# Performance work log

Measured on AMD Instinct MI355X. Metric: run time of the kernel, lower is better.

Reference implementation:

```python
import jax, jax.numpy as jnp
import numpy as np

B, T, C, H = 4, 2048, 768, 12
D = C // H  # head_dim = 64
ROPE_BASE = 10000.0


def _make_rope_cache(seq_len, n_elem, base=ROPE_BASE):
    theta = 1.0 / base ** (jnp.arange(0, n_elem, 2, dtype=jnp.float32) / n_elem)  # [D/2]
    idx_theta = jnp.arange(seq_len, dtype=jnp.float32)[:, None] * theta[None, :]  # [T, D/2]
    return jnp.stack([jnp.cos(idx_theta), jnp.sin(idx_theta)], axis=-1)  # [T, D/2, 2]


def setup_inputs() -> dict:
    key = jax.random.key(0)
    k1, k2, k3 = jax.random.split(key, 3)
    x = jax.random.normal(k1, (B, T, C), dtype=jnp.float32)
    rope_cache = _make_rope_cache(T, D)
    w_qkv = jax.random.normal(k2, (3 * C, C), dtype=jnp.float32) * (1.0 / np.sqrt(C))
    w_o = jax.random.normal(k3, (C, C), dtype=jnp.float32) * (1.0 / np.sqrt(C))
    return {"x": x, "rope_cache": rope_cache, "w_qkv": w_qkv, "w_o": w_o}


def _apply_rope(t, cos, sin):
    # t: [B,T,H,D]; cos/sin: [T,D/2] broadcast to [1,T,1,D/2]
    tp = t.reshape(t.shape[:-1] + (D // 2, 2))
    t0, t1 = tp[..., 0], tp[..., 1]
    c = cos[None, :, None, :]
    s = sin[None, :, None, :]
    rot = jnp.stack([t0 * c - t1 * s, t0 * s + t1 * c], axis=-1)
    return rot.reshape(t.shape)


def reference(x, rope_cache, w_qkv, w_o):
    b, t, c = x.shape
    qkv = (x @ w_qkv.T).reshape(b, t, 3, H, D)
    q, k, v = qkv[:, :, 0], qkv[:, :, 1], qkv[:, :, 2]  # [B,T,H,D]
    cos = rope_cache[:t, :, 0]
    sin = rope_cache[:t, :, 1]
    q = _apply_rope(q, cos, sin)
    k = _apply_rope(k, cos, sin)
    scale = 1.0 / np.sqrt(D)
    att = jnp.einsum('bqhd,bkhd->bhqk', q, k) * scale  # [B,H,T,T]
    causal = jnp.tril(jnp.ones((t, t), dtype=bool))
    att = jnp.where(causal[None, None], att, jnp.finfo(att.dtype).min)
    att = jax.nn.softmax(att, axis=-1)
    y = jnp.einsum('bhqk,bkhd->bqhd', att, v).reshape(b, t, c)
    return y @ w_o.T
```

## Files before the change

kernel.cpp:

```cpp
#include <hip/hip_runtime.h>

#define B_  4
#define T_  2048
#define C_  768
#define H_  12
#define D_  64

typedef unsigned short u16;
typedef unsigned int   u32;
typedef __bf16 bf16;
typedef __bf16 bf16x4 __attribute__((ext_vector_type(4)));
typedef __bf16 bf16x8 __attribute__((ext_vector_type(8)));
typedef float  f32x4  __attribute__((ext_vector_type(4)));
typedef float  f32x16 __attribute__((ext_vector_type(16)));
typedef u32    u32x4  __attribute__((ext_vector_type(4)));
typedef __attribute__((address_space(1))) void* gas_t;
typedef __attribute__((address_space(3))) void* las_t;

static __device__ __forceinline__ u16 f2bf(float f) {
  u32 u = __builtin_bit_cast(u32, f);
  u += 0x7FFFu + ((u >> 16) & 1u);
  return (u16)(u >> 16);
}

static __device__ __forceinline__ u32 cvtpk(float a, float b) {
  u32 r;
  asm("v_cvt_pk_bf16_f32 %0, %1, %2" : "=v"(r) : "v"(a), "v"(b));
  return r;
}
static __device__ __forceinline__ void plswap(u32& a, u32& b) {
  asm volatile("v_permlane32_swap_b32 %0, %1" : "+v"(a), "+v"(b));
}

__global__ __launch_bounds__(256) void k_cvt3(const float* __restrict__ a0,
                                              const float* __restrict__ a1,
                                              const float* __restrict__ a2,
                                              u16* __restrict__ o0,
                                              u16* __restrict__ o1,
                                              u16* __restrict__ o2) {
  const int bid = blockIdx.x;
  const int tid = threadIdx.x;
  if (bid < 6144) {
    const int i = bid * 256 + tid;
    const float4 v = ((const float4*)a0)[i];
    ushort4 o;
    o.x = f2bf(v.x); o.y = f2bf(v.y); o.z = f2bf(v.z); o.w = f2bf(v.w);
    ((ushort4*)o0)[i] = o;
  } else if (bid < 7872) {
    const int i = (bid - 6144) * 256 + tid;
    const int n = i / 192;
    const int c4 = i - n * 192;
    int n2 = n;
    if (n < 1536) {
      const int d = n & 63;
      const int c = (((d & 1) | ((d >> 5) << 1)) << 4) | ((d >> 1) & 15);
      n2 = (n & ~63) | c;
    }
    const float4 v = ((const float4*)a1)[i];
    ushort4 o;
    o.x = f2bf(v.x); o.y = f2bf(v.y); o.z = f2bf(v.z); o.w = f2bf(v.w);
    ((ushort4*)o1)[n2 * 192 + c4] = o;
  } else {
    const int i = (bid - 7872) * 256 + tid;
    const float4 v = ((const float4*)a2)[i];
    ushort4 o;
    o.x = f2bf(v.x); o.y = f2bf(v.y); o.z = f2bf(v.z); o.w = f2bf(v.w);
    ((ushort4*)o2)[i] = o;
  }
}

template<int MODE>
__global__ __launch_bounds__(256) void k_gemm_bt(const u16* __restrict__ A,
                                                 const u16* __restrict__ Bt,
                                                 float* __restrict__ Cout,
                                                 u16* __restrict__ qout,
                                                 u16* __restrict__ kout,
                                                 u16* __restrict__ vout,
                                                 const float* __restrict__ rope,
                                                 int M, int N, int K) {
  __shared__ u16 lA[128 * 32];
  __shared__ u16 lB[128 * 32];
  const int tid = threadIdx.x;
  const int l = tid & 63, w = tid >> 6;
  const int lo = l & 15, hi = l >> 4;
  const int wr = w >> 1, wc = w & 1;
  const int pid = blockIdx.x + gridDim.x * blockIdx.y;
  const int total = gridDim.x * gridDim.y;
  const int lid = (pid & 7) * (total >> 3) + (pid >> 3);
  const int bx = lid % gridDim.x, by = lid / gridDim.x;
  const int m0 = by * 128, n0 = bx * 128;

  f32x4 acc[4][4] = {};
  for (int k0 = 0; k0 < K; k0 += 32) {
#pragma unroll
    for (int r = 0; r < 2; ++r) {
      const int c = tid + 256 * r;
      const int row = c >> 2, cb = (c & 3) * 8;
      __builtin_amdgcn_global_load_lds((gas_t)(u16*)(A + (size_t)(m0 + row) * K + k0 + cb),
                                       (las_t)(lA + c * 8), 16, 0, 0);
      __builtin_amdgcn_global_load_lds((gas_t)(u16*)(Bt + (size_t)(n0 + row) * K + k0 + cb),
                                       (las_t)(lB + c * 8), 16, 0, 0);
    }
    __syncthreads();
    bf16x8 af[4], bfr[4];
#pragma unroll
    for (int i = 0; i < 4; ++i)
      af[i] = *(const bf16x8*)(lA + (wr * 64 + i * 16 + lo) * 32 + hi * 8);
#pragma unroll
    for (int j = 0; j < 4; ++j)
      bfr[j] = *(const bf16x8*)(lB + (wc * 64 + j * 16 + lo) * 32 + hi * 8);
#pragma unroll
    for (int i = 0; i < 4; ++i)
#pragma unroll
      for (int j = 0; j < 4; ++j)
        acc[i][j] = __builtin_amdgcn_mfma_f32_16x16x32_bf16(af[i], bfr[j], acc[i][j], 0, 0, 0);
    __syncthreads();
  }
  const int crow = m0 + wr * 64;
  if (MODE == 1) {
    const int ccol = n0 + wc * 64;
#pragma unroll
    for (int i = 0; i < 4; ++i)
#pragma unroll
      for (int j = 0; j < 4; ++j)
#pragma unroll
        for (int r = 0; r < 4; ++r)
          Cout[(size_t)(crow + i * 16 + hi * 4 + r) * N + ccol + j * 16 + lo] = acc[i][j][r];
  } else {
    const int sect = bx / 6;
    const int h2 = (bx % 6) * 2 + wc;
    if (sect < 2) {
      const float qsc = (sect == 0) ? 0.18033688011f : 1.0f;
      u16* dst = (sect == 0) ? qout : kout;
#pragma unroll
      for (int i = 0; i < 4; ++i)
#pragma unroll
        for (int r = 0; r < 4; ++r) {
          const int trow = crow + i * 16 + hi * 4 + r;
          const int t = trow & (T_ - 1), bb = trow >> 11;
          const float2 cs0 = *(const float2*)(rope + ((size_t)t * 32 + lo) * 2);
          const float2 cs1 = *(const float2*)(rope + ((size_t)t * 32 + 16 + lo) * 2);
          const float a0 = acc[i][0][r], a1 = acc[i][1][r];
          const float a2 = acc[i][2][r], a3 = acc[i][3][r];
          const float e0 = (a0 * cs0.x - a1 * cs0.y) * qsc;
          const float e1 = (a0 * cs0.y + a1 * cs0.x) * qsc;
          const float e2 = (a2 * cs1.x - a3 * cs1.y) * qsc;
          const float e3 = (a2 * cs1.y + a3 * cs1.x) * qsc;
          u16* row = dst + ((size_t)(bb * H_ + h2) * T_ + t) * D_;
          *(ushort2*)(row + 2 * lo)      = make_ushort2(f2bf(e0), f2bf(e1));
          *(ushort2*)(row + 32 + 2 * lo) = make_ushort2(f2bf(e2), f2bf(e3));
        }
    } else {
#pragma unroll
      for (int i = 0; i < 4; ++i)
#pragma unroll
        for (int j = 0; j < 4; ++j)
#pragma unroll
          for (int r = 0; r < 4; ++r) {
            const int trow = crow + i * 16 + hi * 4 + r;
            vout[(size_t)trow * C_ + h2 * D_ + j * 16 + lo] = f2bf(acc[i][j][r]);
          }
    }
  }
}

__global__ __launch_bounds__(256) void k_vtrans(const u16* __restrict__ vtmp,
                                                u16* __restrict__ vt) {
  __shared__ u16 lds[64][68];
  const int bid = blockIdx.x;
  const int ttile = bid & 31, bh = bid >> 5;
  const int b = bh / H_, h = bh % H_;
  const int tid = threadIdx.x;
  const int tl = tid >> 2, doff = (tid & 3) * 16;
  const u16* src = vtmp + (size_t)(b * T_ + ttile * 64 + tl) * C_ + h * D_ + doff;
  const uint4 v0 = *(const uint4*)(src);
  const uint4 v1 = *(const uint4*)(src + 8);
  *(uint2*)&lds[tl][doff + 0]  = make_uint2(v0.x, v0.y);
  *(uint2*)&lds[tl][doff + 4]  = make_uint2(v0.z, v0.w);
  *(uint2*)&lds[tl][doff + 8]  = make_uint2(v1.x, v1.y);
  *(uint2*)&lds[tl][doff + 12] = make_uint2(v1.z, v1.w);
  __syncthreads();
  const int d = tl, toff = doff;
  uint4 o0, o1;
#define PK(j) ((u32)lds[toff + (j)][d] | ((u32)lds[toff + (j) + 1][d] << 16))
  o0.x = PK(0);  o0.y = PK(2);  o0.z = PK(4);  o0.w = PK(6);
  o1.x = PK(8);  o1.y = PK(10); o1.z = PK(12); o1.w = PK(14);
#undef PK
  u16* dst = vt + ((size_t)bh * D_ + d) * T_ + ttile * 64 + toff;
  *(uint4*)(dst) = o0;
  *(uint4*)(dst + 8) = o1;
}

__global__ __launch_bounds__(256) void k_attn(const u16* __restrict__ qb,
                                              const u16* __restrict__ kb,
                                              const u16* __restrict__ vtb,
                                              u16* __restrict__ yb) {
  __shared__ u16 kbuf[2][64 * 64];
  __shared__ u16 vbuf[2][64 * 64];
  const int tid = threadIdx.x;
  const int w = tid >> 6, l = tid & 63;
  const int q5 = l & 31, hf = l >> 5;
  const int pid = blockIdx.x;
  const int xcd = pid & 7;
  const int rank = pid >> 3;
  const int wv = rank >> 5, ps = rank & 31;
  const int widx = wv * 32 + ((wv & 1) ? 31 - ps : ps);
  const int bh_local = widx % 6;
  const int bx = 15 - widx / 6;
  const int bh = xcd * 6 + bh_local;
  const int h = bh % H_, b = bh / H_;
  const u16* Q  = qb  + (size_t)bh * T_ * D_;
  const u16* K  = kb  + (size_t)bh * T_ * D_;
  const u16* Vt = vtb + (size_t)bh * D_ * T_;
  const int nt = 2 * bx + 2;
  const int q0w = bx * 128 + w * 32;
  const int q = q0w + q5;

  const int srow = tid >> 3;
  const int scb  = ((tid & 7) * 16) ^ ((srow & 7) << 4);

#define STAGE(bufi, j0s)                                                             \
  do {                                                                               \
    __builtin_amdgcn_global_load_lds((gas_t)(u16*)(K + (size_t)((j0s) + srow) * D_ + (scb >> 1)),      \
                                     (las_t)(&kbuf[bufi][0] + tid * 8), 16, 0, 0);   \
    __builtin_amdgcn_global_load_lds((gas_t)(u16*)(K + (size_t)((j0s) + 32 + srow) * D_ + (scb >> 1)), \
                                     (las_t)(&kbuf[bufi][0] + (tid + 256) * 8), 16, 0, 0);             \
    __builtin_amdgcn_global_load_lds((gas_t)(u16*)(Vt + (size_t)srow * T_ + (j0s) + (scb >> 1)),       \
                                     (las_t)(&vbuf[bufi][0] + tid * 8), 16, 0, 0);   \
    __builtin_amdgcn_global_load_lds((gas_t)(u16*)(Vt + (size_t)(32 + srow) * T_ + (j0s) + (scb >> 1)),\
                                     (las_t)(&vbuf[bufi][0] + (tid + 256) * 8), 16, 0, 0);             \
  } while (0)

  bf16x8 qf[4];
#pragma unroll
  for (int dc = 0; dc < 4; ++dc)
    qf[dc] = *(const bf16x8*)(Q + (size_t)q * D_ + dc * 16 + hf * 8);

  const f32x16 Z = {};
  f32x16 o0 = {}, o1 = {};
  float ls0 = 0.f, ls1 = 0.f, ls2 = 0.f, ls3 = 0.f;

  STAGE(0, 0);
  asm volatile("s_waitcnt vmcnt(0)" ::: "memory");
  __builtin_amdgcn_s_barrier();
  __builtin_amdgcn_sched_barrier(0);
  int cur = 0;
  for (int t = 0; t < nt; ++t) {
    const int j0 = t * 64;
    if (t + 1 < nt) {
      STAGE(cur ^ 1, (t + 1) * 64);
      asm volatile("s_waitcnt vmcnt(4)" ::: "memory");
    } else {
      asm volatile("s_waitcnt vmcnt(0)" ::: "memory");
    }
    __builtin_amdgcn_s_barrier();
    __builtin_amdgcn_sched_barrier(0);
    if (j0 <= q0w + 31) {
      const u16* kb_l = &kbuf[cur][0];
      const u16* vb_l = &vbuf[cur][0];
      const int swz = (l & 7) << 4;
#pragma unroll
      for (int st = 0; st < 2; ++st) {
        f32x16 s;
        __builtin_amdgcn_s_setprio(1);
        {
          const int krow = st * 32 + q5;
          const bf16x8 kd0 = *(const bf16x8*)(kb_l + krow * 64 + (((0   + 16 * hf) ^ swz) >> 1));
          s = __builtin_amdgcn_mfma_f32_32x32x16_bf16(kd0, qf[0], Z, 0, 0, 0);
          const bf16x8 kd1 = *(const bf16x8*)(kb_l + krow * 64 + (((32  + 16 * hf) ^ swz) >> 1));
          s = __builtin_amdgcn_mfma_f32_32x32x16_bf16(kd1, qf[1], s, 0, 0, 0);
          const bf16x8 kd2 = *(const bf16x8*)(kb_l + krow * 64 + (((64  + 16 * hf) ^ swz) >> 1));
          s = __builtin_amdgcn_mfma_f32_32x32x16_bf16(kd2, qf[2], s, 0, 0, 0);
          const bf16x8 kd3 = *(const bf16x8*)(kb_l + krow * 64 + (((96  + 16 * hf) ^ swz) >> 1));
          s = __builtin_amdgcn_mfma_f32_32x32x16_bf16(kd3, qf[3], s, 0, 0, 0);
        }
        __builtin_amdgcn_s_setprio(0);
        if (j0 + 63 > q0w) {
#pragma unroll
          for (int r = 0; r < 16; ++r) {
            const int kv = j0 + 32 * st + (r & 3) + 8 * (r >> 2) + 4 * hf;
            if (kv > q) s[r] = -1e30f;
          }
        }
#pragma unroll
        for (int r = 0; r < 16; ++r)
          s[r] = __builtin_amdgcn_exp2f(s[r]);
#pragma unroll
        for (int r = 0; r < 16; r += 4) {
          ls0 += s[r];
          ls1 += s[r + 1];
          ls2 += s[r + 2];
          ls3 += s[r + 3];
        }
        u32 a0 = cvtpk(s[0],  s[1]),  b0 = cvtpk(s[4],  s[5]);  plswap(a0, b0);
        u32 a1 = cvtpk(s[2],  s[3]),  b1 = cvtpk(s[6],  s[7]);  plswap(a1, b1);
        u32 a2 = cvtpk(s[8],  s[9]),  b2 = cvtpk(s[12], s[13]); plswap(a2, b2);
        u32 a3 = cvtpk(s[10], s[11]), b3 = cvtpk(s[14], s[15]); plswap(a3, b3);
        const bf16x8 pa0 = __builtin_bit_cast(bf16x8, (u32x4){a0, a1, b0, b1});
        const bf16x8 pa1 = __builtin_bit_cast(bf16x8, (u32x4){a2, a3, b2, b3});
        __builtin_amdgcn_s_setprio(1);
        {
          const int ks0 = st * 2, ks1 = st * 2 + 1;
          const bf16x8 vf00 = *(const bf16x8*)(vb_l + q5 * 64        + (((ks0 * 32 + 16 * hf) ^ swz) >> 1));
          const bf16x8 vf10 = *(const bf16x8*)(vb_l + (32 + q5) * 64 + (((ks0 * 32 + 16 * hf) ^ swz) >> 1));
          o0 = __builtin_amdgcn_mfma_f32_32x32x16_bf16(vf00, pa0, o0, 0, 0, 0);
          o1 = __builtin_amdgcn_mfma_f32_32x32x16_bf16(vf10, pa0, o1, 0, 0, 0);
          const bf16x8 vf01 = *(const bf16x8*)(vb_l + q5 * 64        + (((ks1 * 32 + 16 * hf) ^ swz) >> 1));
          const bf16x8 vf11 = *(const bf16x8*)(vb_l + (32 + q5) * 64 + (((ks1 * 32 + 16 * hf) ^ swz) >> 1));
          o0 = __builtin_amdgcn_mfma_f32_32x32x16_bf16(vf01, pa1, o0, 0, 0, 0);
          o1 = __builtin_amdgcn_mfma_f32_32x32x16_bf16(vf11, pa1, o1, 0, 0, 0);
        }
        __builtin_amdgcn_s_setprio(0);
      }
    }
    asm volatile("" ::: "memory");
    __builtin_amdgcn_s_barrier();
    __builtin_amdgcn_sched_barrier(0);
    cur ^= 1;
  }
#undef STAGE
  const float lsum = (ls0 + ls1) + (ls2 + ls3);
  const float lt = lsum + __shfl_xor(lsum, 32);
  const float linv = 1.0f / lt;
  u16* yrow = yb + (size_t)(b * T_ + q) * C_ + h * D_;
#pragma unroll
  for (int g = 0; g < 4; ++g) {
    bf16x4 ok0, ok1;
#pragma unroll
    for (int r = 0; r < 4; ++r) {
      ok0[r] = (__bf16)(o0[4 * g + r] * linv);
      ok1[r] = (__bf16)(o1[4 * g + r] * linv);
    }
    *(bf16x4*)(yrow + g * 8 + 4 * hf)      = ok0;
    *(bf16x4*)(yrow + 32 + g * 8 + 4 * hf) = ok1;
  }
}

extern "C" void kernel_launch(void* const* d_in, const int* in_sizes, int n_in,
                              void* d_out, int out_size, void* d_ws, size_t ws_size,
                              hipStream_t stream) {
  (void)in_sizes; (void)n_in; (void)out_size; (void)ws_size;
  const float* x    = (const float*)d_in[0];
  const float* rope = (const float*)d_in[1];
  const float* wqkv = (const float*)d_in[2];
  const float* wo   = (const float*)d_in[3];
  float* out = (float*)d_out;
  char* ws = (char*)d_ws;
  u16* xb    = (u16*)(ws);
  u16* wqkvb = (u16*)(ws + 12582912);
  u16* wob   = (u16*)(ws + 16121856);
  u16* vtmp  = (u16*)(ws + 17301504);
  u16* qb    = (u16*)(ws + 55050240);
  u16* kb    = (u16*)(ws + 67633152);
  u16* vtb   = (u16*)(ws + 80216064);
  u16* yb    = xb;

  k_cvt3<<<8448, 256, 0, stream>>>(x, wqkv, wo, xb, wqkvb, wob);
  k_gemm_bt<2><<<dim3(18, 64), 256, 0, stream>>>(xb, wqkvb, nullptr, qb, kb, vtmp,
                                                 rope, 8192, 2304, 768);
  k_vtrans<<<1536, 256, 0, stream>>>(vtmp, vtb);
  k_attn<<<768, 256, 0, stream>>>(qb, kb, vtb, yb);
  k_gemm_bt<1><<<dim3(6, 64), 256, 0, stream>>>(yb, wob, out, nullptr, nullptr, nullptr,
                                                nullptr, 8192, 768, 768);
}
```

Before: 143.7 us.

## Rework GEMM with BK=64 swizzled LDS, double buffering, and smaller output-projection tiles

The GEMM kernel now stages 64-wide K slices into LDS with an XOR swizzle that avoids bank conflicts. It raises MFMA issue priority with setprio and replaces __syncthreads with explicit waitcnt and barriers. The output projection uses 64-row tiles with double-buffered prefetch and a doubled grid, so the small-N GEMM fills more CUs. The cost is more LDS per block and hand-written waitcnt counts that must match the number of loads issued per stage.

```diff
diff --git a/kernel.cpp b/kernel.cpp
--- a/kernel.cpp
+++ b/kernel.cpp
@@ -69,7 +69,7 @@
   }
 }
 
-template<int MODE>
+template<int MODE, int BM>
 __global__ __launch_bounds__(256) void k_gemm_bt(const u16* __restrict__ A,
                                                  const u16* __restrict__ Bt,
                                                  float* __restrict__ Cout,
@@ -78,55 +78,107 @@
                                                  u16* __restrict__ vout,
                                                  const float* __restrict__ rope,
                                                  int M, int N, int K) {
-  __shared__ u16 lA[128 * 32];
-  __shared__ u16 lB[128 * 32];
+  constexpr int NJ = (BM == 128) ? 4 : 2;
+  constexpr int PA = BM / 32;
+  constexpr int NB = (BM == 64) ? 2 : 1;
+  __shared__ u16 lA[NB * BM * 64];
+  __shared__ u16 lB[NB * 128 * 64];
   const int tid = threadIdx.x;
   const int l = tid & 63, w = tid >> 6;
   const int lo = l & 15, hi = l >> 4;
-  const int wr = w >> 1, wc = w & 1;
+  const int wrow = (BM == 128) ? (w >> 1) * 64 : 0;
+  const int wcol = (BM == 128) ? (w & 1) * 64 : w * 32;
   const int pid = blockIdx.x + gridDim.x * blockIdx.y;
   const int total = gridDim.x * gridDim.y;
   const int lid = (pid & 7) * (total >> 3) + (pid >> 3);
   const int bx = lid % gridDim.x, by = lid / gridDim.x;
-  const int m0 = by * 128, n0 = bx * 128;
-
-  f32x4 acc[4][4] = {};
-  for (int k0 = 0; k0 < K; k0 += 32) {
-#pragma unroll
-    for (int r = 0; r < 2; ++r) {
-      const int c = tid + 256 * r;
-      const int row = c >> 2, cb = (c & 3) * 8;
-      __builtin_amdgcn_global_load_lds((gas_t)(u16*)(A + (size_t)(m0 + row) * K + k0 + cb),
-                                       (las_t)(lA + c * 8), 16, 0, 0);
-      __builtin_amdgcn_global_load_lds((gas_t)(u16*)(Bt + (size_t)(n0 + row) * K + k0 + cb),
-                                       (las_t)(lB + c * 8), 16, 0, 0);
-    }
-    __syncthreads();
-    bf16x8 af[4], bfr[4];
+  const int m0 = by * BM, n0 = bx * 128;
+
+  const int srow_t = tid >> 3;
+  const int scb   = ((tid & 7) * 16) ^ ((srow_t & 7) << 4);
+  const int swz   = (lo & 7) << 4;
+
+  auto STAGE = [&](int bufi, int k0) {
+#pragma unroll
+    for (int p = 0; p < PA; ++p)
+      __builtin_amdgcn_global_load_lds(
+          (gas_t)(u16*)(A + (size_t)(m0 + srow_t + 32 * p) * K + k0 + (scb >> 1)),
+          (las_t)(lA + bufi * BM * 64 + p * 2048 + tid * 8), 16, 0, 0);
+#pragma unroll
+    for (int p = 0; p < 4; ++p)
+      __builtin_amdgcn_global_load_lds(
+          (gas_t)(u16*)(Bt + (size_t)(n0 + srow_t + 32 * p) * K + k0 + (scb >> 1)),
+          (las_t)(lB + bufi * 128 * 64 + p * 2048 + tid * 8), 16, 0, 0);
+  };
+
+  f32x4 acc[4][NJ] = {};
+  auto COMPUTE = [&](const u16* la, const u16* lb) {
+#pragma unroll
+    for (int kk = 0; kk < 2; ++kk) {
+      const int co = ((kk * 64 + hi * 16) ^ swz) >> 1;
+      bf16x8 af[4], bfr[NJ];
+#pragma unroll
+      for (int i = 0; i < 4; ++i)
+        af[i] = *(const bf16x8*)(la + (wrow + i * 16 + lo) * 64 + co);
+#pragma unroll
+      for (int j = 0; j < NJ; ++j)
+        bfr[j] = *(const bf16x8*)(lb + (wcol + j * 16 + lo) * 64 + co);
+      __builtin_amdgcn_s_setprio(1);
+#pragma unroll
+      for (int i = 0; i < 4; ++i)
+#pragma unroll
+        for (int j = 0; j < NJ; ++j)
+          acc[i][j] = __builtin_amdgcn_mfma_f32_16x16x32_bf16(af[i], bfr[j], acc[i][j], 0, 0, 0);
+      __builtin_amdgcn_s_setprio(0);
+    }
+  };
+
+  if (BM == 128) {
+    for (int k0 = 0; k0 < K; k0 += 64) {
+      STAGE(0, k0);
+      asm volatile("s_waitcnt vmcnt(0)" ::: "memory");
+      __builtin_amdgcn_s_barrier();
+      __builtin_amdgcn_sched_barrier(0);
+      COMPUTE(lA, lB);
+      asm volatile("" ::: "memory");
+      __builtin_amdgcn_s_barrier();
+      __builtin_amdgcn_sched_barrier(0);
+    }
+  } else {
+    STAGE(0, 0);
+    asm volatile("s_waitcnt vmcnt(0)" ::: "memory");
+    __builtin_amdgcn_s_barrier();
+    __builtin_amdgcn_sched_barrier(0);
+    int cur = 0;
+    const int nk = K >> 6;
+    for (int ks = 0; ks < nk; ++ks) {
+      if (ks + 1 < nk) {
+        STAGE(cur ^ 1, (ks + 1) * 64);
+        asm volatile("s_waitcnt vmcnt(6)" ::: "memory");
+      } else {
+        asm volatile("s_waitcnt vmcnt(0)" ::: "memory");
+      }
+      __builtin_amdgcn_s_barrier();
+      __builtin_amdgcn_sched_barrier(0);
+      COMPUTE(lA + cur * BM * 64, lB + cur * 128 * 64);
+      asm volatile("" ::: "memory");
+      __builtin_amdgcn_s_barrier();
+      __builtin_amdgcn_sched_barrier(0);
+      cur ^= 1;
+    }
+  }
+
+  const int crow = m0 + wrow;
+  if (MODE == 1) {
 #pragma unroll
     for (int i = 0; i < 4; ++i)
-      af[i] = *(const bf16x8*)(lA + (wr * 64 + i * 16 + lo) * 32 + hi * 8);
-#pragma unroll
-    for (int j = 0; j < 4; ++j)
-      bfr[j] = *(const bf16x8*)(lB + (wc * 64 + j * 16 + lo) * 32 + hi * 8);
-#pragma unroll
-    for (int i = 0; i < 4; ++i)
-#pragma unroll
-      for (int j = 0; j < 4; ++j)
-        acc[i][j] = __builtin_amdgcn_mfma_f32_16x16x32_bf16(af[i], bfr[j], acc[i][j], 0, 0, 0);
-    __syncthreads();
-  }
-  const int crow = m0 + wr * 64;
-  if (MODE == 1) {
-    const int ccol = n0 + wc * 64;
-#pragma unroll
-    for (int i = 0; i < 4; ++i)
-#pragma unroll
-      for (int j = 0; j < 4; ++j)
+#pragma unroll
+      for (int j = 0; j < NJ; ++j)
 #pragma unroll
         for (int r = 0; r < 4; ++r)
-          Cout[(size_t)(crow + i * 16 + hi * 4 + r) * N + ccol + j * 16 + lo] = acc[i][j][r];
+          Cout[(size_t)(crow + i * 16 + hi * 4 + r) * N + n0 + wcol + j * 16 + lo] = acc[i][j][r];
   } else {
+    const int wc = w & 1;
     const int sect = bx / 6;
     const int h2 = (bx % 6) * 2 + wc;
     if (sect < 2) {
@@ -154,7 +206,7 @@
 #pragma unroll
       for (int i = 0; i < 4; ++i)
 #pragma unroll
-        for (int j = 0; j < 4; ++j)
+        for (int j = 0; j < NJ; ++j)
 #pragma unroll
           for (int r = 0; r < 4; ++r) {
             const int trow = crow + i * 16 + hi * 4 + r;
@@ -356,10 +408,10 @@
   u16* yb    = xb;
 
   k_cvt3<<<8448, 256, 0, stream>>>(x, wqkv, wo, xb, wqkvb, wob);
-  k_gemm_bt<2><<<dim3(18, 64), 256, 0, stream>>>(xb, wqkvb, nullptr, qb, kb, vtmp,
-                                                 rope, 8192, 2304, 768);
+  k_gemm_bt<2, 128><<<dim3(18, 64), 256, 0, stream>>>(xb, wqkvb, nullptr, qb, kb, vtmp,
+                                                      rope, 8192, 2304, 768);
   k_vtrans<<<1536, 256, 0, stream>>>(vtmp, vtb);
   k_attn<<<768, 256, 0, stream>>>(qb, kb, vtb, yb);
-  k_gemm_bt<1><<<dim3(6, 64), 256, 0, stream>>>(yb, wob, out, nullptr, nullptr, nullptr,
-                                                nullptr, 8192, 768, 768);
-}
+  k_gemm_bt<1, 64><<<dim3(6, 128), 256, 0, stream>>>(yb, wob, out, nullptr, nullptr, nullptr,
+                                                     nullptr, 8192, 768, 768);
+}
```

Result: faster. 127.4 us (-11.3%).
